# Optimization experiments

Measured on AMD Instinct MI355X. Metric: run time of the kernel, lower is better.

Reference implementation:

```python
import jax, jax.numpy as jnp
import numpy as np

# dims: batch, points, patches(groups), patch size, hidden, heads, layers, ffn
B, N, G, K, D, H, L, F = 32, 8192, 256, 32, 384, 6, 12, 1536
MASK_RATIO = 0.75
LEN_KEEP = int(G * (1 - MASK_RATIO))  # 64 visible tokens
HD = D // H


def _layernorm(x, g, b, eps=1e-5):
    m = jnp.mean(x, -1, keepdims=True)
    v = jnp.mean(jnp.square(x - m), -1, keepdims=True)
    return (x - m) * jax.lax.rsqrt(v + eps) * g + b


def _normalize_points(x):
    # normalize(): center = mid of bbox, radius = max distance to center (iso/diag)
    bmin = x.min(-2, keepdims=True)
    bmax = x.max(-2, keepdims=True)
    center = 0.5 * (bmin + bmax)
    radius = jnp.linalg.norm(x - center, axis=-1, keepdims=True).max(-2, keepdims=True)
    return (x - center) / radius


def _fps(x, num_samples):
    # farthest point sampling; sequential by nature -> fori_loop over G (fixed, small)
    b, n, _ = x.shape
    idxs = jnp.zeros((b, num_samples), jnp.int32)

    def body(i, state):
        dists, idxs, last = state
        lastpt = jnp.take_along_axis(x, last[:, None, None].astype(jnp.int32), axis=1)  # [B,1,3]
        d = jnp.sum(jnp.square(x - lastpt), -1)  # [B,N]
        dists = jnp.minimum(dists, d)
        nxt = jnp.argmax(dists, -1).astype(jnp.int32)
        return dists, idxs.at[:, i].set(nxt), nxt

    dists0 = jnp.full((b, n), 1e10, x.dtype)
    _, idxs, _ = jax.lax.fori_loop(1, num_samples, body, (dists0, idxs, jnp.zeros((b,), jnp.int32)))
    return idxs


def _group(x, centers):
    # squared pairwise distances without materializing [B,G,N,3]
    d2 = (jnp.sum(jnp.square(centers), -1)[:, :, None]
          + jnp.sum(jnp.square(x), -1)[:, None, :]
          - 2.0 * jnp.einsum('bgc,bnc->bgn', centers, x))  # [B,G,N]
    _, idx = jax.lax.top_k(-d2, K)  # [B,G,K] knn indices
    nbrs = jnp.take_along_axis(x[:, None, :, :], idx[..., None], axis=2)  # [B,G,K,3] (_knn_gather)
    return nbrs - centers[:, :, None, :]


def setup_inputs() -> dict:
    key = jax.random.key(0)
    ks = iter(jax.random.split(key, 24))

    def w(shape, scale=0.02):
        return jax.random.normal(next(ks), shape, jnp.float32) * scale

    ones_ln = jnp.stack([jnp.ones(D, jnp.float32), jnp.zeros(D, jnp.float32)])
    return {
        'points': jax.random.normal(next(ks), (B, N, 3), jnp.float32),
        'noise': jax.random.uniform(next(ks), (B, G), jnp.float32),
        # mini-PointNet patch encoder
        'pe_w1': w((3, 128)), 'pe_b1': jnp.zeros((128,), jnp.float32),
        'pe_w2': w((128, 256)), 'pe_b2': jnp.zeros((256,), jnp.float32),
        'pe_w3': w((256, D)), 'pe_b3': jnp.zeros((D,), jnp.float32),
        # positional MLP on patch centers
        'pos_w1': w((3, 128)), 'pos_b1': jnp.zeros((128,), jnp.float32),
        'pos_w2': w((128, D)), 'pos_b2': jnp.zeros((D,), jnp.float32),
        # transformer (stacked over L layers)
        'ln1': jnp.tile(ones_ln[None], (L, 1, 1)),
        'wqkv': w((L, D, 3 * D)), 'bqkv': jnp.zeros((L, 3 * D), jnp.float32),
        'wo': w((L, D, D)), 'bo': jnp.zeros((L, D), jnp.float32),
        'ln2': jnp.tile(ones_ln[None], (L, 1, 1)),
        'wi': w((L, D, F)), 'bi': jnp.zeros((L, F), jnp.float32),
        'wo2': w((L, F, D)), 'bo2': jnp.zeros((L, D), jnp.float32),
        'lnf': ones_ln,
    }


def _forward(points, noise, pe_w1, pe_b1, pe_w2, pe_b2, pe_w3, pe_b3,
             pos_w1, pos_b1, pos_w2, pos_b2,
             ln1, wqkv, bqkv, wo, bo, ln2, wi, bi, wo2, bo2, lnf):
    x = _normalize_points(points)
    cidx = _fps(x, G)                                        # [B,G]
    centers = jnp.take_along_axis(x, cidx[..., None], axis=1)  # [B,G,3]
    patches = _group(x, centers)                              # [B,G,K,3]

    # patch encode (per-point MLP -> max pool -> proj)
    f = jax.nn.relu(patches @ pe_w1 + pe_b1)
    f = f @ pe_w2 + pe_b2
    tokens = f.max(axis=2) @ pe_w3 + pe_b3                    # [B,G,D]
    pos = jax.nn.relu(centers @ pos_w1 + pos_b1) @ pos_w2 + pos_b2  # [B,G,D]

    # mask(): argsort-of-noise shuffle, keep first len_keep tokens
    ids_shuffle = jnp.argsort(noise, axis=1)
    ids_keep = ids_shuffle[:, :LEN_KEEP]                      # [B,64]
    h = (jnp.take_along_axis(tokens, ids_keep[..., None], axis=1)
         + jnp.take_along_axis(pos, ids_keep[..., None], axis=1))  # [B,64,D]

    scale = 1.0 / jnp.sqrt(jnp.asarray(HD, h.dtype))

    def layer(h, p):
        l1, wq, bq, wo_, bo_, l2, wi_, bi_, wo2_, bo2_ = p
        y = _layernorm(h, l1[0], l1[1])
        qkv = (y @ wq + bq).reshape(B, LEN_KEEP, 3, H, HD)  # '(three h d)' split
        q, k, v = jnp.moveaxis(qkv, 2, 0)
        a = jax.nn.softmax(jnp.einsum('bshd,bthd->bhst', q, k) * scale, -1)
        o = jnp.einsum('bhst,bthd->bshd', a, v).reshape(B, LEN_KEEP, D)
        h = h + o @ wo_ + bo_
        y = _layernorm(h, l2[0], l2[1])
        h = h + jax.nn.gelu(y @ wi_ + bi_) @ wo2_ + bo2_
        return h, None

    h, _ = jax.lax.scan(layer, h, (ln1, wqkv, bqkv, wo, bo, ln2, wi, bi, wo2, bo2))
    return _layernorm(h, lnf[0], lnf[1])


def reference(points, noise, pe_w1, pe_b1, pe_w2, pe_b2, pe_w3, pe_b3,
              pos_w1, pos_b1, pos_w2, pos_b2,
              ln1, wqkv, bqkv, wo, bo, ln2, wi, bi, wo2, bo2, lnf):
    return _forward(points, noise, pe_w1, pe_b1, pe_w2, pe_b2, pe_w3, pe_b3,
                    pos_w1, pos_b1, pos_w2, pos_b2,
                    ln1, wqkv, bqkv, wo, bo, ln2, wi, bi, wo2, bo2, lnf)
```

## Files before the change

### kernel.cpp

```cpp
#include <hip/hip_runtime.h>

#define NPTS 8192
#define NB   32
#define NG   256
#define NK   32
#define ND   384
#define NH   6
#define NLK  64
#define NF   1536
#define NHD  64
#define NL   12
#define MM   2048

typedef unsigned short u16;
typedef unsigned long long u64;
typedef __attribute__((ext_vector_type(8))) short short8;
typedef __attribute__((ext_vector_type(16))) float f32x16;
typedef __attribute__((ext_vector_type(4))) unsigned short ushort4v;

#define PL_PRE   147456ull
#define PL_LAYER 1769472ull
#define WT_ELEMS (PL_PRE + 12ull*PL_LAYER)

__device__ __forceinline__ float bf2f(u16 v){
  unsigned int u = ((unsigned int)v) << 16;
  float f; __builtin_memcpy(&f, &u, 4); return f;
}
__device__ __forceinline__ float ldf(const void* p, size_t i, bool bf){
  if(bf) return bf2f(((const u16*)p)[i]);
  return ((const float*)p)[i];
}
__device__ __forceinline__ u16 f2bf(float f){
  unsigned int x; __builtin_memcpy(&x, &f, 4);
  x += 0x7fffu + ((x >> 16) & 1u);
  return (u16)(x >> 16);
}
__device__ __forceinline__ void split2(float v, u16& hi, u16& lo){
  hi = f2bf(v);
  lo = f2bf(v - bf2f(hi));
}

__device__ __forceinline__ float blockMax256(float v, float* sb, int tid){
  for(int off=32; off; off>>=1) v = fmaxf(v, __shfl_down(v, off));
  __syncthreads();
  if((tid&63)==0) sb[tid>>6] = v;
  __syncthreads();
  return fmaxf(fmaxf(sb[0],sb[1]), fmaxf(sb[2],sb[3]));
}

__global__ __launch_bounds__(256) void k_normalize(const void* __restrict__ pts,
                                                   float* __restrict__ xn,
                                                   int* __restrict__ flag){
#pragma clang fp contract(off)
  int b = blockIdx.x, tid = threadIdx.x;
  __shared__ float sb[4];
  __shared__ int sbad;
  if(tid==0) sbad = 0;
  __syncthreads();
  {
    const u16* p16 = (const u16*)pts;
    int hit=0;
    for(int i=tid; i<4096; i+=256){
      unsigned e = (p16[i] >> 7) & 0xFFu;
      if(e >= 0x90u) hit=1;
    }
    if(hit) atomicOr(&sbad, 1);
  }
  __syncthreads();
  const bool bf = (sbad == 0);
  if(b==0 && tid==0) flag[0] = bf ? 1 : 0;
  const size_t base = (size_t)b*NPTS*3;
  float mn0=1e30f,mn1=1e30f,mn2=1e30f, mx0=-1e30f,mx1=-1e30f,mx2=-1e30f;
  for(int n=tid; n<NPTS; n+=256){
    float x0=ldf(pts,base+n*3,bf), x1=ldf(pts,base+n*3+1,bf), x2=ldf(pts,base+n*3+2,bf);
    mn0=fminf(mn0,x0); mx0=fmaxf(mx0,x0);
    mn1=fminf(mn1,x1); mx1=fmaxf(mx1,x1);
    mn2=fminf(mn2,x2); mx2=fmaxf(mx2,x2);
  }
  mx0=blockMax256(mx0,sb,tid); mn0=-blockMax256(-mn0,sb,tid);
  mx1=blockMax256(mx1,sb,tid); mn1=-blockMax256(-mn1,sb,tid);
  mx2=blockMax256(mx2,sb,tid); mn2=-blockMax256(-mn2,sb,tid);
  float c0=0.5f*(mn0+mx0), c1=0.5f*(mn1+mx1), c2=0.5f*(mn2+mx2);
  float mr=0.0f;
  for(int n=tid; n<NPTS; n+=256){
    float d0=ldf(pts,base+n*3,bf)-c0, d1=ldf(pts,base+n*3+1,bf)-c1, d2=ldf(pts,base+n*3+2,bf)-c2;
    float nr = sqrtf((d0*d0 + d1*d1) + d2*d2);
    mr = fmaxf(mr, nr);
  }
  float radius = blockMax256(mr, sb, tid);
  float* XO = xn + base;
  for(int n=tid; n<NPTS; n+=256){
    XO[n*3  ] = (ldf(pts,base+n*3  ,bf)-c0)/radius;
    XO[n*3+1] = (ldf(pts,base+n*3+1,bf)-c1)/radius;
    XO[n*3+2] = (ldf(pts,base+n*3+2,bf)-c2)/radius;
  }
}

__device__ __forceinline__ void kmax_dpp_step(unsigned& hi, unsigned& lo, unsigned oh, unsigned ol){
  bool g = (oh > hi) || (oh == hi && ol > lo);
  hi = g ? oh : hi; lo = g ? ol : lo;
}
#define KMAX_DPP(CTRL) { \
  unsigned oh=(unsigned)__builtin_amdgcn_update_dpp(0,(int)kh,(CTRL),0xf,0xf,true); \
  unsigned ol=(unsigned)__builtin_amdgcn_update_dpp(0,(int)kl,(CTRL),0xf,0xf,true); \
  kmax_dpp_step(kh,kl,oh,ol); }

__global__ __launch_bounds__(512) void k_fps_trans(
    const float* __restrict__ xn, float* __restrict__ centers,
    const void* __restrict__ noise, int* __restrict__ keep,
    const void* __restrict__ pe_w3, const void* __restrict__ pos_w2,
    const void* __restrict__ wqkv, const void* __restrict__ wo,
    const void* __restrict__ wi,   const void* __restrict__ wo2,
    u16* __restrict__ wthi, u16* __restrict__ wtlo,
    const int* __restrict__ flag)
{
  __shared__ float xs[NPTS*3];
  __shared__ u64 skey[3];
  __shared__ int sc[NG];
  int tid = threadIdx.x;

  if(blockIdx.x >= 64){
    const bool bf = flag[0]!=0;
    float (*t)[33] = reinterpret_cast<float(*)[33]>(xs);
    int gid = blockIdx.x - 64;
    const void* W; int Kd, Nd; size_t woff, doff; int local;
    if(gid < 96){        W=pe_w3;  Kd=256; Nd=384; woff=0; doff=0;      local=gid; }
    else if(gid < 144){  W=pos_w2; Kd=128; Nd=384; woff=0; doff=98304;  local=gid-96; }
    else{
      int g2 = gid - 144; int l = g2 / 1728; int id = g2 % 1728;
      size_t lb = PL_PRE + (size_t)l*PL_LAYER;
      if(id < 432){        W=wqkv; Kd=384;  Nd=1152; woff=(size_t)l*442368; doff=lb;          local=id; }
      else if(id < 576){   W=wo;   Kd=384;  Nd=384;  woff=(size_t)l*147456; doff=lb+442368;   local=id-432; }
      else if(id < 1152){  W=wi;   Kd=384;  Nd=1536; woff=(size_t)l*589824; doff=lb+589824;   local=id-576; }
      else {               W=wo2;  Kd=1536; Nd=384;  woff=(size_t)l*589824; doff=lb+1179648;  local=id-1152; }
    }
    int ntiles = Nd >> 5;
    int n0 = (local % ntiles)*32, k0 = (local / ntiles)*32;
    for(int i=0;i<2;i++){
      int idx = tid + i*512; int kr = idx>>5, nc = idx&31;
      t[kr][nc] = ldf(W, woff + (size_t)(k0+kr)*Nd + n0+nc, bf);
    }
    __syncthreads();
    for(int i=0;i<2;i++){
      int idx = tid + i*512; int nr = idx>>5, kc = idx&31;
      float v = t[kc][nr];
      u16 hi,lo; split2(v,hi,lo);
      size_t o = doff + (size_t)(n0+nr)*Kd + k0+kc;
      wthi[o]=hi; wtlo[o]=lo;
    }
    return;
  }

  if(blockIdx.x >= 32){
    const bool bf = flag[0]!=0;
    int b = blockIdx.x - 32;
    float* nv = xs;
    if(tid < NG) nv[tid] = ldf(noise, (size_t)b*NG+tid, bf);
    __syncthreads();
    if(tid < NG){
      float v = nv[tid]; int r = 0;
      for(int j=0; j<NG; j++){
        float u = nv[j];
        r += (u < v) || (u == v && j < tid);
      }
      if(r < NLK) keep[b*NLK + r] = tid;
    }
    return;
  }

  {
#pragma clang fp contract(off)
    int b = blockIdx.x;
    int lane = tid & 63;
    const float* X = xn + (size_t)b*NPTS*3;
    float px[16],py[16],pz[16],dd[16];
#pragma unroll
    for(int s=0;s<16;s++){
      int n = s*512 + tid;
      px[s]=X[n*3]; py[s]=X[n*3+1]; pz[s]=X[n*3+2];
      dd[s]=1e10f;
    }
    for(int i=tid; i<NPTS*3; i+=512) xs[i] = X[i];
    if(tid==0){ skey[0]=0ull; skey[1]=0ull; skey[2]=0ull; sc[0]=0; }
    __syncthreads();
    float lx = xs[0], ly = xs[1], lz = xs[2];
    for(int i=1;i<NG;i++){
      int c = i % 3;
      float bv=-1.0f; int bs=0;
#pragma unroll
      for(int s=0;s<16;s++){
        float dx=px[s]-lx, dy=py[s]-ly, dz=pz[s]-lz;
        float d=(dx*dx + dy*dy) + dz*dz;
        d = fminf(dd[s], d); dd[s]=d;
        if(d > bv){ bv=d; bs=s; }
      }
      int bn = bs*512 + tid;
      unsigned kh; __builtin_memcpy(&kh,&bv,4);
      unsigned kl = (unsigned)(NPTS-1-bn);
      KMAX_DPP(0x111)
      KMAX_DPP(0x112)
      KMAX_DPP(0x114)
      KMAX_DPP(0x118)
      KMAX_DPP(0x142)
      KMAX_DPP(0x143)
      if(lane==63) atomicMax(&skey[c], ((u64)kh<<32) | (u64)kl);
      __syncthreads();
      u64 k64 = skey[c];
      int n = (NPTS-1) - (int)(k64 & 0xFFFFFFFFull);
      n &= (NPTS-1);
      if(tid==0){ sc[i]=n; skey[(i+2)%3]=0ull; }
      lx = xs[n*3]; ly = xs[n*3+1]; lz = xs[n*3+2];
    }
    __syncthreads();
    if(tid < NG){
      int n = sc[tid] & (NPTS-1);
      centers[((size_t)b*NG+tid)*3  ] = xs[n*3];
      centers[((size_t)b*NG+tid)*3+1] = xs[n*3+1];
      centers[((size_t)b*NG+tid)*3+2] = xs[n*3+2];
    }
  }
}

__global__ __launch_bounds__(256) void k_knn(
    const float* __restrict__ xn, const float* __restrict__ centers,
    const int* __restrict__ keep, float* __restrict__ patches)
{
  int blk=blockIdx.x; int b=blk>>6; int j=blk&63; int tid=threadIdx.x;
  __shared__ float sd[NPTS];
  __shared__ int   sel[NK];
  __shared__ float rv[4]; __shared__ int rn[4];
  __shared__ int   sseln;
  int g = keep[b*NLK + j] & (NG-1);
  const float* C = centers + ((size_t)b*NG + g)*3;
  float c0=C[0], c1=C[1], c2=C[2];
  const float* X = xn + (size_t)b*NPTS*3;
  {
#pragma clang fp contract(off)
    float cc = (c0*c0 + c1*c1) + c2*c2;
    for(int n=tid; n<NPTS; n+=256){
      float x0=X[n*3], x1=X[n*3+1], x2=X[n*3+2];
      float xx=(x0*x0 + x1*x1) + x2*x2;
      float dt=(c0*x0 + c1*x1) + c2*x2;
      sd[n] = (cc + xx) - 2.0f*dt;
    }
  }
  __syncthreads();
  float dl[32];
  for(int s=0;s<32;s++) dl[s] = sd[s*256 + tid];
  unsigned int alive = 0xffffffffu;
  for(int r=0; r<NK; r++){
    float bv=1e30f; int bn=0x7fffffff;
    for(int s=0;s<32;s++){
      if(alive & (1u<<s)){
        float v = dl[s];
        if(v < bv){ bv=v; bn=s*256+tid; }
      }
    }
    for(int off=32;off;off>>=1){
      float ov=__shfl_down(bv,off); int on=__shfl_down(bn,off);
      if(ov<bv || (ov==bv && on<bn)){ bv=ov; bn=on; }
    }
    if((tid&63)==0){ rv[tid>>6]=bv; rn[tid>>6]=bn; }
    __syncthreads();
    if(tid==0){
      float v=rv[0]; int n=rn[0];
      for(int w=1;w<4;w++) if(rv[w]<v || (rv[w]==v && rn[w]<n)){ v=rv[w]; n=rn[w]; }
      n &= (NPTS-1);
      sseln=n; sel[r]=n;
    }
    __syncthreads();
    int n = sseln;
    if((n & 255) == tid) alive &= ~(1u << (n >> 8));
  }
  __syncthreads();
  if(tid < NK){
    int n = sel[tid] & (NPTS-1);
    float* P = patches + ((size_t)(b*NLK+j)*NK + tid)*3;
    P[0]=X[n*3  ]-c0;
    P[1]=X[n*3+1]-c1;
    P[2]=X[n*3+2]-c2;
  }
}

__global__ __launch_bounds__(256) void k_embed(
    const float* __restrict__ patches, const float* __restrict__ centers,
    const int* __restrict__ keep,
    const void* __restrict__ w1, const void* __restrict__ b1,
    const void* __restrict__ w2, const void* __restrict__ b2,
    const void* __restrict__ pw1, const void* __restrict__ pb1,
    u16* __restrict__ mfhi, u16* __restrict__ mflo,
    u16* __restrict__ phhi, u16* __restrict__ phlo,
    const int* __restrict__ flag)
{
  int blk=blockIdx.x; int b=blk>>6; int j=blk&63; int tid=threadIdx.x;
  const bool bf = flag[0] != 0;
  __shared__ float pat[NK*3];
  __shared__ __align__(16) float f1t[128*36];
  int row = b*NLK + j;
  if(tid < NK*3) pat[tid] = patches[(size_t)row*NK*3 + tid];
  __syncthreads();
  for(int i=0;i<16;i++){
    int idx = tid + i*256;
    int k = idx>>7, m = idx&127;
    float v = ldf(b1,m,bf)
            + pat[k*3+0]*ldf(w1,        m,bf)
            + pat[k*3+1]*ldf(w1, 128 + m,bf)
            + pat[k*3+2]*ldf(w1, 256 + m,bf);
    f1t[m*36 + k] = fmaxf(v, 0.0f);
  }
  __syncthreads();
  float acc[NK];
  {
    float bv = ldf(b2, tid, bf);
#pragma unroll
    for(int k=0;k<NK;k++) acc[k]=bv;
  }
  for(int jj=0;jj<128;jj++){
    float wv = ldf(w2, (size_t)jj*256+tid, bf);
    const float* fr = &f1t[jj*36];
#pragma unroll
    for(int k8=0;k8<8;k8++){
      float4 fv = *reinterpret_cast<const float4*>(fr + k8*4);
      acc[k8*4+0] = fmaf(fv.x, wv, acc[k8*4+0]);
      acc[k8*4+1] = fmaf(fv.y, wv, acc[k8*4+1]);
      acc[k8*4+2] = fmaf(fv.z, wv, acc[k8*4+2]);
      acc[k8*4+3] = fmaf(fv.w, wv, acc[k8*4+3]);
    }
  }
  float mx = acc[0];
#pragma unroll
  for(int k=1;k<NK;k++) mx = fmaxf(mx, acc[k]);
  { u16 hi,lo; split2(mx,hi,lo);
    mfhi[(size_t)row*256 + tid]=hi; mflo[(size_t)row*256 + tid]=lo; }
  if(tid < 128){
    int g = keep[b*NLK + j] & (NG-1);
    const float* C = centers + ((size_t)b*NG + g)*3;
    float v = ldf(pb1,tid,bf)
            + C[0]*ldf(pw1,        tid,bf)
            + C[1]*ldf(pw1, 128 + tid,bf)
            + C[2]*ldf(pw1, 256 + tid,bf);
    v = fmaxf(v, 0.0f);
    u16 hi,lo; split2(v,hi,lo);
    phhi[(size_t)row*128 + tid]=hi; phlo[(size_t)row*128 + tid]=lo;
  }
}

__global__ __launch_bounds__(256) void k_transpose4(
    const void* __restrict__ wqkv, const void* __restrict__ wo,
    const void* __restrict__ wi,   const void* __restrict__ wo2,
    int l, u16* __restrict__ dhi, u16* __restrict__ dlo,
    const int* __restrict__ flag){
  __shared__ float t[32][33];
  const bool bf = flag[0]!=0;
  int id = blockIdx.x;
  const void* W; int Kd, Nd; size_t woff, doff; int local;
  if(id < 432){        W=wqkv; Kd=384;  Nd=1152; woff=(size_t)l*442368; doff=PL_PRE;          local=id; }
  else if(id < 576){   W=wo;   Kd=384;  Nd=384;  woff=(size_t)l*147456; doff=PL_PRE+442368;   local=id-432; }
  else if(id < 1152){  W=wi;   Kd=384;  Nd=1536; woff=(size_t)l*589824; doff=PL_PRE+589824;   local=id-576; }
  else {               W=wo2;  Kd=1536; Nd=384;  woff=(size_t)l*589824; doff=PL_PRE+1179648;  local=id-1152; }
  int ntiles = Nd >> 5;
  int n0 = (local % ntiles)*32, k0 = (local / ntiles)*32;
  for(int i=0;i<4;i++){
    int idx = threadIdx.x + i*256; int kr = idx>>5, nc = idx&31;
    t[kr][nc] = ldf(W, woff + (size_t)(k0+kr)*Nd + n0+nc, bf);
  }
  __syncthreads();
  for(int i=0;i<4;i++){
    int idx = threadIdx.x + i*256; int nr = idx>>5, kc = idx&31;
    float v = t[kc][nr];
    u16 hi,lo; split2(v,hi,lo);
    size_t o = doff + (size_t)(n0+nr)*Kd + k0+kc;
    dhi[o]=hi; dlo[o]=lo;
  }
}

__global__ __launch_bounds__(128) void k_ln_split(const float* __restrict__ X,
                                                  const void* __restrict__ gb, size_t go,
                                                  u16* __restrict__ Yhi, u16* __restrict__ Ylo,
                                                  const int* __restrict__ flag){
  int row=blockIdx.x, tid=threadIdx.x;
  const bool bf = flag[0] != 0;
  const float* x = X + (size_t)row*ND;
  __shared__ float sbuf[2];
  float v0=x[tid], v1=x[tid+128], v2=x[tid+256];
  float s = v0+v1+v2;
  for(int off=32;off;off>>=1) s += __shfl_down(s,off);
  if((tid&63)==0) sbuf[tid>>6]=s;
  __syncthreads();
  float mean = (sbuf[0]+sbuf[1]) * (1.0f/(float)ND);
  __syncthreads();
  float d0=v0-mean, d1=v1-mean, d2=v2-mean;
  s = d0*d0 + d1*d1 + d2*d2;
  for(int off=32;off;off>>=1) s += __shfl_down(s,off);
  if((tid&63)==0) sbuf[tid>>6]=s;
  __syncthreads();
  float var = (sbuf[0]+sbuf[1]) * (1.0f/(float)ND);
  float rstd = 1.0f / sqrtf(var + 1e-5f);
  float o0 = d0*rstd*ldf(gb,go+tid    ,bf) + ldf(gb,go+ND+tid    ,bf);
  float o1 = d1*rstd*ldf(gb,go+tid+128,bf) + ldf(gb,go+ND+tid+128,bf);
  float o2 = d2*rstd*ldf(gb,go+tid+256,bf) + ldf(gb,go+ND+tid+256,bf);
  u16 hi,lo; size_t rb = (size_t)row*ND;
  split2(o0,hi,lo); Yhi[rb+tid    ]=hi; Ylo[rb+tid    ]=lo;
  split2(o1,hi,lo); Yhi[rb+tid+128]=hi; Ylo[rb+tid+128]=lo;
  split2(o2,hi,lo); Yhi[rb+tid+256]=hi; Ylo[rb+tid+256]=lo;
}

template<int TM, int TN, int ACT, bool RES, bool OSPLIT>
__global__ __launch_bounds__(256) void k_gemm_mfma(
    const u16* __restrict__ Ahi, const u16* __restrict__ Alo,
    const u16* __restrict__ Whi, const u16* __restrict__ Wlo, size_t wo,
    const void* __restrict__ bias, size_t bo, const int* __restrict__ flag,
    const float* __restrict__ res, float* __restrict__ Cf,
    u16* __restrict__ Ohi, u16* __restrict__ Olo,
    int N, int K)
{
  __shared__ __align__(16) u16 sAh[2][64*40];
  __shared__ __align__(16) u16 sAl[2][64*40];
  __shared__ __align__(16) u16 sBh[2][64*40];
  __shared__ __align__(16) u16 sBl[2][64*40];
  int tid = threadIdx.x;
  int wave = tid >> 6, lane = tid & 63;
  int wm = wave >> 1, wn = wave & 1;
  int l31 = lane & 31, half = lane >> 5;
  int row0 = blockIdx.y*TM, col0 = blockIdx.x*TN;
  const bool bf = flag[0] != 0;
  f32x16 acc;
#pragma unroll
  for(int r=0;r<16;r++) acc[r]=0.f;

  const int sr  = tid >> 2;
  const int scc = (tid & 3) * 8;
  const u16* gAh = Ahi + (size_t)(row0+sr)*K + scc;
  const u16* gAl = Alo + (size_t)(row0+sr)*K + scc;
  const u16* gBh = Whi + wo + (size_t)(col0+sr)*K + scc;
  const u16* gBl = Wlo + wo + (size_t)(col0+sr)*K + scc;
  const int ldst = sr*40 + scc;

  uint4 rah = *reinterpret_cast<const uint4*>(gAh);
  uint4 ral = *reinterpret_cast<const uint4*>(gAl);
  uint4 rbh = *reinterpret_cast<const uint4*>(gBh);
  uint4 rbl = *reinterpret_cast<const uint4*>(gBl);

  const int nk = K >> 5;
  for(int t=0; t<nk; ++t){
    const int buf = t & 1;
    *reinterpret_cast<uint4*>(&sAh[buf][ldst]) = rah;
    *reinterpret_cast<uint4*>(&sAl[buf][ldst]) = ral;
    *reinterpret_cast<uint4*>(&sBh[buf][ldst]) = rbh;
    *reinterpret_cast<uint4*>(&sBl[buf][ldst]) = rbl;
    __syncthreads();
    if(t+1 < nk){
      const int ko = (t+1) << 5;
      rah = *reinterpret_cast<const uint4*>(gAh + ko);
      ral = *reinterpret_cast<const uint4*>(gAl + ko);
      rbh = *reinterpret_cast<const uint4*>(gBh + ko);
      rbl = *reinterpret_cast<const uint4*>(gBl + ko);
    }
#pragma unroll
    for(int ks=0; ks<2; ks++){
      int aoff = (wm*32 + l31)*40 + ks*16 + half*8;
      int boff = (wn*32 + l31)*40 + ks*16 + half*8;
      short8 ah = *reinterpret_cast<const short8*>(&sAh[buf][aoff]);
      short8 al = *reinterpret_cast<const short8*>(&sAl[buf][aoff]);
      short8 bh = *reinterpret_cast<const short8*>(&sBh[buf][boff]);
      short8 bl = *reinterpret_cast<const short8*>(&sBl[buf][boff]);
      acc = __builtin_amdgcn_mfma_f32_32x32x16_bf16(ah, bh, acc, 0,0,0);
      acc = __builtin_amdgcn_mfma_f32_32x32x16_bf16(ah, bl, acc, 0,0,0);
      acc = __builtin_amdgcn_mfma_f32_32x32x16_bf16(al, bh, acc, 0,0,0);
    }
  }
  int col = col0 + wn*32 + l31;
  float bv = ldf(bias, bo+col, bf);
#pragma unroll
  for(int r=0;r<16;r++){
    int row = row0 + wm*32 + (r&3) + 8*(r>>2) + 4*half;
    float v = acc[r] + bv;
    if(ACT==1){
      float xx = v;
      v = 0.5f*xx*(1.0f + tanhf(0.7978845608028654f*(xx + 0.044715f*xx*xx*xx)));
    }
    if(RES) v += res[(size_t)row*N + col];
    if(OSPLIT){
      u16 hi,lo; split2(v,hi,lo);
      Ohi[(size_t)row*N + col]=hi; Olo[(size_t)row*N + col]=lo;
    }else{
      Cf[(size_t)row*N + col]=v;
    }
  }
}

__global__ __launch_bounds__(256) void k_attn_pl(const float* __restrict__ qkv,
                                                 u16* __restrict__ ohi,
                                                 u16* __restrict__ olo){
  __shared__ float Qt[64*68];
  __shared__ float Kt[64*68];
  __shared__ float V [64*68];
  __shared__ float SB[64*68];
  int blk=blockIdx.x; int b=blk/NH, h=blk%NH;
  int tid=threadIdx.x;
  for(int idx=tid; idx<4096; idx+=256){
    int s=idx>>6, d=idx&63;
    const float* r = qkv + ((size_t)(b*NLK+s))*1152 + h*NHD + d;
    Qt[d*68+s]=r[0];
    Kt[d*68+s]=r[384];
    V [s*68+d]=r[768];
  }
  __syncthreads();
  {
    const int i0 = (tid>>4)*4, j0 = (tid&15)*4;
    float a00=0.f,a01=0.f,a02=0.f,a03=0.f;
    float a10=0.f,a11=0.f,a12=0.f,a13=0.f;
    float a20=0.f,a21=0.f,a22=0.f,a23=0.f;
    float a30=0.f,a31=0.f,a32=0.f,a33=0.f;
#pragma unroll 4
    for(int d=0;d<64;d++){
      float4 qa = *reinterpret_cast<const float4*>(&Qt[d*68+i0]);
      float4 kb = *reinterpret_cast<const float4*>(&Kt[d*68+j0]);
      a00=fmaf(qa.x,kb.x,a00); a01=fmaf(qa.x,kb.y,a01); a02=fmaf(qa.x,kb.z,a02); a03=fmaf(qa.x,kb.w,a03);
      a10=fmaf(qa.y,kb.x,a10); a11=fmaf(qa.y,kb.y,a11); a12=fmaf(qa.y,kb.z,a12); a13=fmaf(qa.y,kb.w,a13);
      a20=fmaf(qa.z,kb.x,a20); a21=fmaf(qa.z,kb.y,a21); a22=fmaf(qa.z,kb.z,a22); a23=fmaf(qa.z,kb.w,a23);
      a30=fmaf(qa.w,kb.x,a30); a31=fmaf(qa.w,kb.y,a31); a32=fmaf(qa.w,kb.z,a32); a33=fmaf(qa.w,kb.w,a33);
    }
    float4 o0 = {a00*0.125f, a01*0.125f, a02*0.125f, a03*0.125f};
    float4 o1 = {a10*0.125f, a11*0.125f, a12*0.125f, a13*0.125f};
    float4 o2 = {a20*0.125f, a21*0.125f, a22*0.125f, a23*0.125f};
    float4 o3 = {a30*0.125f, a31*0.125f, a32*0.125f, a33*0.125f};
    *reinterpret_cast<float4*>(&SB[(i0  )*68+j0]) = o0;
    *reinterpret_cast<float4*>(&SB[(i0+1)*68+j0]) = o1;
    *reinterpret_cast<float4*>(&SB[(i0+2)*68+j0]) = o2;
    *reinterpret_cast<float4*>(&SB[(i0+3)*68+j0]) = o3;
  }
  __syncthreads();
  if(tid<64){
    float* rowp=&SB[tid*68];
    float m=rowp[0];
    for(int j=1;j<64;j++) m=fmaxf(m,rowp[j]);
    float sum=0.0f;
    for(int j=0;j<64;j++){ float e=__expf(rowp[j]-m); rowp[j]=e; sum+=e; }
    for(int j=0;j<64;j++) Qt[j*68+tid] = rowp[j]/sum;
  }
  __syncthreads();
  {
    const int s0 = (tid>>4)*4, d0 = (tid&15)*4;
    float a00=0.f,a01=0.f,a02=0.f,a03=0.f;
    float a10=0.f,a11=0.f,a12=0.f,a13=0.f;
    float a20=0.f,a21=0.f,a22=0.f,a23=0.f;
    float a30=0.f,a31=0.f,a32=0.f,a33=0.f;
#pragma unroll 4
    for(int t=0;t<64;t++){
      float4 av = *reinterpret_cast<const float4*>(&Qt[t*68+s0]);
      float4 vv = *reinterpret_cast<const float4*>(&V [t*68+d0]);
      a00=fmaf(av.x,vv.x,a00); a01=fmaf(av.x,vv.y,a01); a02=fmaf(av.x,vv.z,a02); a03=fmaf(av.x,vv.w,a03);
      a10=fmaf(av.y,vv.x,a10); a11=fmaf(av.y,vv.y,a11); a12=fmaf(av.y,vv.z,a12); a13=fmaf(av.y,vv.w,a13);
      a20=fmaf(av.z,vv.x,a20); a21=fmaf(av.z,vv.y,a21); a22=fmaf(av.z,vv.z,a22); a23=fmaf(av.z,vv.w,a23);
      a30=fmaf(av.w,vv.x,a30); a31=fmaf(av.w,vv.y,a31); a32=fmaf(av.w,vv.z,a32); a33=fmaf(av.w,vv.w,a33);
    }
    float rr[4][4] = {{a00,a01,a02,a03},{a10,a11,a12,a13},{a20,a21,a22,a23},{a30,a31,a32,a33}};
#pragma unroll
    for(int si=0; si<4; si++){
      ushort4v h4, l4;
#pragma unroll
      for(int di=0; di<4; di++){
        u16 hi,lo; split2(rr[si][di],hi,lo);
        h4[di]=hi; l4[di]=lo;
      }
      size_t o = ((size_t)(b*NLK+s0+si))*ND + h*NHD + d0;
      *reinterpret_cast<ushort4v*>(&ohi[o]) = h4;
      *reinterpret_cast<ushort4v*>(&olo[o]) = l4;
    }
  }
}

template<bool FINAL>
__global__ __launch_bounds__(128) void k_ln(const float* __restrict__ X,
                                            const void* __restrict__ gb, size_t go,
                                            void* __restrict__ Y,
                                            const int* __restrict__ flag){
  int row=blockIdx.x, tid=threadIdx.x;
  const bool bf = flag[0] != 0;
  const float* x = X + (size_t)row*ND;
  __shared__ float sbuf[2];
  float v0=x[tid], v1=x[tid+128], v2=x[tid+256];
  float s = v0+v1+v2;
  for(int off=32;off;off>>=1) s += __shfl_down(s,off);
  if((tid&63)==0) sbuf[tid>>6]=s;
  __syncthreads();
  float mean = (sbuf[0]+sbuf[1]) * (1.0f/(float)ND);
  __syncthreads();
  float d0=v0-mean, d1=v1-mean, d2=v2-mean;
  s = d0*d0 + d1*d1 + d2*d2;
  for(int off=32;off;off>>=1) s += __shfl_down(s,off);
  if((tid&63)==0) sbuf[tid>>6]=s;
  __syncthreads();
  float var = (sbuf[0]+sbuf[1]) * (1.0f/(float)ND);
  float rstd = 1.0f / sqrtf(var + 1e-5f);
  float o0 = d0*rstd*ldf(gb,go+tid    ,bf) + ldf(gb,go+ND+tid    ,bf);
  float o1 = d1*rstd*ldf(gb,go+tid+128,bf) + ldf(gb,go+ND+tid+128,bf);
  float o2 = d2*rstd*ldf(gb,go+tid+256,bf) + ldf(gb,go+ND+tid+256,bf);
  if(FINAL && bf){
    u16* yo = (u16*)Y + (size_t)row*ND;
    yo[tid]=f2bf(o0); yo[tid+128]=f2bf(o1); yo[tid+256]=f2bf(o2);
  }else{
    float* yo = (float*)Y + (size_t)row*ND;
    yo[tid]=o0; yo[tid+128]=o1; yo[tid+256]=o2;
  }
}

extern "C" void kernel_launch(void* const* d_in, const int* in_sizes, int n_in,
                              void* d_out, int out_size, void* d_ws, size_t ws_size,
                              hipStream_t stream){
  (void)in_sizes; (void)n_in; (void)out_size;
  const void* pts   = d_in[0];
  const void* noise = d_in[1];
  const void* pe_w1 = d_in[2];
  const void* pe_b1 = d_in[3];
  const void* pe_w2 = d_in[4];
  const void* pe_b2 = d_in[5];
  const void* pe_w3 = d_in[6];
  const void* pe_b3 = d_in[7];
  const void* pos_w1= d_in[8];
  const void* pos_b1= d_in[9];
  const void* pos_w2= d_in[10];
  const void* pos_b2= d_in[11];
  const void* ln1   = d_in[12];
  const void* wqkv  = d_in[13];
  const void* bqkv  = d_in[14];
  const void* wo    = d_in[15];
  const void* bo    = d_in[16];
  const void* ln2   = d_in[17];
  const void* wi    = d_in[18];
  const void* bi    = d_in[19];
  const void* wo2   = d_in[20];
  const void* bo2   = d_in[21];
  const void* lnf   = d_in[22];

  const size_t needed_small = (6711296ull + 16) * 4;
  if (ws_size < needed_small) return;
  const size_t wt_f32_off = 6711312ull;
  const size_t needed_big = (wt_f32_off + WT_ELEMS) * 4;
  const bool big = ws_size >= needed_big;

  float* ws   = (float*)d_ws;
  float* h    = ws;
  u16*  yhi   = (u16*)(ws + 786432);
  u16*  ylo   = yhi + 786432;
  float* qkvb = ws + 1572864;
  u16*  athi  = (u16*)(ws + 3932160);
  u16*  atlo  = athi + 786432;
  u16*  ubhi  = (u16*)(ws + 1572864);
  u16*  ublo  = ubhi + 3145728;
  float* xn   = ws + 1572864;
  float* patches;
  float* centers;
  int*   keep;
  int*   flag;
  u16 *wthi, *wtlo;
  if(big){
    patches = ws + 6488064;
    centers = ws + 6684672;
    keep    = (int*)(ws + 6709248);
    flag    = (int*)(ws + 6711296);
    wthi    = (u16*)(ws + wt_f32_off);
    wtlo    = wthi + WT_ELEMS;
  }else{
    wthi    = (u16*)(ws + 4718592);
    wtlo    = (u16*)(ws + 5677056);
    patches = ws + 6635520;
    centers = ws + 6832128;
    keep    = (int*)(ws + 6856704);
    flag    = (int*)(ws + 6858752);
    if(ws_size < (6858752ull + 16) * 4) return;
  }

  k_normalize<<<NB, 256, 0, stream>>>(pts, xn, flag);
  {
    int grid = big ? (64 + 144 + 12*1728) : (64 + 144);
    k_fps_trans<<<grid, 512, 0, stream>>>(xn, centers, noise, keep, pe_w3, pos_w2,
        wqkv, wo, wi, wo2, wthi, wtlo, flag);
  }
  k_knn      <<<NB*NLK, 256, 0, stream>>>(xn, centers, keep, patches);
  k_embed    <<<NB*NLK, 256, 0, stream>>>(patches, centers, keep,
      pe_w1, pe_b1, pe_w2, pe_b2, pos_w1, pos_b1,
      yhi , yhi + 2048*256 , athi , athi + 2048*128 , flag);
  k_gemm_mfma<64,64,0,false,false><<<dim3(6,32), 256, 0, stream>>>(
      yhi, yhi + 2048*256, wthi, wtlo, 0, pe_b3, 0, flag, nullptr, h, nullptr, nullptr, 384, 256);
  k_gemm_mfma<64,64,0,true ,false><<<dim3(6,32), 256, 0, stream>>>(
      athi, athi + 2048*128, wthi, wtlo, 98304, pos_b2, 0, flag, h, h, nullptr, nullptr, 384, 128);

  for(int l=0; l<NL; l++){
    size_t lb = big ? (PL_PRE + (size_t)l*PL_LAYER) : PL_PRE;
    if(!big){
      k_transpose4<<<1728, 256, 0, stream>>>(wqkv, wo, wi, wo2, l, wthi, wtlo, flag);
    }
    k_ln_split<<<MM, 128, 0, stream>>>(h, ln1, (size_t)l*2*ND, yhi, ylo, flag);
    k_gemm_mfma<64,64,0,false,false><<<dim3(18,32), 256, 0, stream>>>(
        yhi, ylo, wthi, wtlo, lb, bqkv, (size_t)l*1152, flag, nullptr, qkvb, nullptr, nullptr, 1152, 384);
    k_attn_pl<<<NB*NH, 256, 0, stream>>>(qkvb, athi, atlo);
    k_gemm_mfma<64,64,0,true ,false><<<dim3(6,32), 256, 0, stream>>>(
        athi, atlo, wthi, wtlo, lb + 442368, bo, (size_t)l*384, flag, h, h, nullptr, nullptr, 384, 384);
    k_ln_split<<<MM, 128, 0, stream>>>(h, ln2, (size_t)l*2*ND, yhi, ylo, flag);
    k_gemm_mfma<64,64,1,false,true ><<<dim3(24,32), 256, 0, stream>>>(
        yhi, ylo, wthi, wtlo, lb + 589824, bi, (size_t)l*1536, flag, nullptr, nullptr, ubhi, ublo, 1536, 384);
    k_gemm_mfma<64,64,0,true ,false><<<dim3(6,32), 256, 0, stream>>>(
        ubhi, ublo, wthi, wtlo, lb + 1179648, bo2, (size_t)l*384, flag, h, h, nullptr, nullptr, 384, 1536);
  }
  k_ln<true><<<MM, 128, 0, stream>>>(h, lnf, 0, d_out, flag);
}
```

Baseline: 1.804 ms.

## Fuse kNN with patch embedding and double-register prefetch in GEMM

Merges the kNN selection and the first patch-embedding MLP into one kernel. The gathered patch stays in shared memory and the distance buffer is reused for the hidden activations, which removes a launch and a global round trip. Separately, the MFMA GEMM main loop is unrolled by two with two register sets of prefetched tiles, so global loads run two k-steps ahead. That costs extra registers and assumes the k-step count is even.

Measured after the change: 1.695 ms. -6.1%, faster.

```diff
diff --git a/kernel.cpp b/kernel.cpp
--- a/kernel.cpp
+++ b/kernel.cpp
@@ -221,15 +221,23 @@
   }
 }
 
-__global__ __launch_bounds__(256) void k_knn(
+__global__ __launch_bounds__(256) void k_knn_embed(
     const float* __restrict__ xn, const float* __restrict__ centers,
-    const int* __restrict__ keep, float* __restrict__ patches)
+    const int* __restrict__ keep,
+    const void* __restrict__ w1, const void* __restrict__ b1,
+    const void* __restrict__ w2, const void* __restrict__ b2,
+    const void* __restrict__ pw1, const void* __restrict__ pb1,
+    u16* __restrict__ mfhi, u16* __restrict__ mflo,
+    u16* __restrict__ phhi, u16* __restrict__ phlo,
+    const int* __restrict__ flag)
 {
   int blk=blockIdx.x; int b=blk>>6; int j=blk&63; int tid=threadIdx.x;
-  __shared__ float sd[NPTS];
+  const bool bf = flag[0] != 0;
+  __shared__ __align__(16) float sd[NPTS];
   __shared__ int   sel[NK];
   __shared__ float rv[4]; __shared__ int rn[4];
   __shared__ int   sseln;
+  __shared__ float pat[NK*3];
   int g = keep[b*NLK + j] & (NG-1);
   const float* C = centers + ((size_t)b*NG + g)*3;
   float c0=C[0], c1=C[1], c2=C[2];
@@ -275,30 +283,13 @@
   __syncthreads();
   if(tid < NK){
     int n = sel[tid] & (NPTS-1);
-    float* P = patches + ((size_t)(b*NLK+j)*NK + tid)*3;
-    P[0]=X[n*3  ]-c0;
-    P[1]=X[n*3+1]-c1;
-    P[2]=X[n*3+2]-c2;
-  }
-}
-
-__global__ __launch_bounds__(256) void k_embed(
-    const float* __restrict__ patches, const float* __restrict__ centers,
-    const int* __restrict__ keep,
-    const void* __restrict__ w1, const void* __restrict__ b1,
-    const void* __restrict__ w2, const void* __restrict__ b2,
-    const void* __restrict__ pw1, const void* __restrict__ pb1,
-    u16* __restrict__ mfhi, u16* __restrict__ mflo,
-    u16* __restrict__ phhi, u16* __restrict__ phlo,
-    const int* __restrict__ flag)
-{
-  int blk=blockIdx.x; int b=blk>>6; int j=blk&63; int tid=threadIdx.x;
-  const bool bf = flag[0] != 0;
-  __shared__ float pat[NK*3];
-  __shared__ __align__(16) float f1t[128*36];
+    pat[tid*3+0] = X[n*3  ]-c0;
+    pat[tid*3+1] = X[n*3+1]-c1;
+    pat[tid*3+2] = X[n*3+2]-c2;
+  }
+  __syncthreads();
+  float* f1t = sd;
   int row = b*NLK + j;
-  if(tid < NK*3) pat[tid] = patches[(size_t)row*NK*3 + tid];
-  __syncthreads();
   for(int i=0;i<16;i++){
     int idx = tid + i*256;
     int k = idx>>7, m = idx&127;
@@ -333,12 +324,10 @@
   { u16 hi,lo; split2(mx,hi,lo);
     mfhi[(size_t)row*256 + tid]=hi; mflo[(size_t)row*256 + tid]=lo; }
   if(tid < 128){
-    int g = keep[b*NLK + j] & (NG-1);
-    const float* C = centers + ((size_t)b*NG + g)*3;
     float v = ldf(pb1,tid,bf)
-            + C[0]*ldf(pw1,        tid,bf)
-            + C[1]*ldf(pw1, 128 + tid,bf)
-            + C[2]*ldf(pw1, 256 + tid,bf);
+            + c0*ldf(pw1,        tid,bf)
+            + c1*ldf(pw1, 128 + tid,bf)
+            + c2*ldf(pw1, 256 + tid,bf);
     v = fmaxf(v, 0.0f);
     u16 hi,lo; split2(v,hi,lo);
     phhi[(size_t)row*128 + tid]=hi; phlo[(size_t)row*128 + tid]=lo;
@@ -436,39 +425,50 @@
   const u16* gBl = Wlo + wo + (size_t)(col0+sr)*K + scc;
   const int ldst = sr*40 + scc;
 
-  uint4 rah = *reinterpret_cast<const uint4*>(gAh);
-  uint4 ral = *reinterpret_cast<const uint4*>(gAl);
-  uint4 rbh = *reinterpret_cast<const uint4*>(gBh);
-  uint4 rbl = *reinterpret_cast<const uint4*>(gBl);
+  uint4 rah0 = *reinterpret_cast<const uint4*>(gAh);
+  uint4 ral0 = *reinterpret_cast<const uint4*>(gAl);
+  uint4 rbh0 = *reinterpret_cast<const uint4*>(gBh);
+  uint4 rbl0 = *reinterpret_cast<const uint4*>(gBl);
+  uint4 rah1 = *reinterpret_cast<const uint4*>(gAh + 32);
+  uint4 ral1 = *reinterpret_cast<const uint4*>(gAl + 32);
+  uint4 rbh1 = *reinterpret_cast<const uint4*>(gBh + 32);
+  uint4 rbl1 = *reinterpret_cast<const uint4*>(gBl + 32);
 
   const int nk = K >> 5;
-  for(int t=0; t<nk; ++t){
-    const int buf = t & 1;
-    *reinterpret_cast<uint4*>(&sAh[buf][ldst]) = rah;
-    *reinterpret_cast<uint4*>(&sAl[buf][ldst]) = ral;
-    *reinterpret_cast<uint4*>(&sBh[buf][ldst]) = rbh;
-    *reinterpret_cast<uint4*>(&sBl[buf][ldst]) = rbl;
-    __syncthreads();
-    if(t+1 < nk){
-      const int ko = (t+1) << 5;
-      rah = *reinterpret_cast<const uint4*>(gAh + ko);
-      ral = *reinterpret_cast<const uint4*>(gAl + ko);
-      rbh = *reinterpret_cast<const uint4*>(gBh + ko);
-      rbl = *reinterpret_cast<const uint4*>(gBl + ko);
-    }
-#pragma unroll
-    for(int ks=0; ks<2; ks++){
-      int aoff = (wm*32 + l31)*40 + ks*16 + half*8;
-      int boff = (wn*32 + l31)*40 + ks*16 + half*8;
-      short8 ah = *reinterpret_cast<const short8*>(&sAh[buf][aoff]);
-      short8 al = *reinterpret_cast<const short8*>(&sAl[buf][aoff]);
-      short8 bh = *reinterpret_cast<const short8*>(&sBh[buf][boff]);
-      short8 bl = *reinterpret_cast<const short8*>(&sBl[buf][boff]);
-      acc = __builtin_amdgcn_mfma_f32_32x32x16_bf16(ah, bh, acc, 0,0,0);
-      acc = __builtin_amdgcn_mfma_f32_32x32x16_bf16(ah, bl, acc, 0,0,0);
-      acc = __builtin_amdgcn_mfma_f32_32x32x16_bf16(al, bh, acc, 0,0,0);
-    }
-  }
+
+#define GEMM_STEP(S, TT) { \
+    *reinterpret_cast<uint4*>(&sAh[S][ldst]) = rah##S; \
+    *reinterpret_cast<uint4*>(&sAl[S][ldst]) = ral##S; \
+    *reinterpret_cast<uint4*>(&sBh[S][ldst]) = rbh##S; \
+    *reinterpret_cast<uint4*>(&sBl[S][ldst]) = rbl##S; \
+    __syncthreads(); \
+    if((TT)+2 < nk){ \
+      const int ko = ((TT)+2) << 5; \
+      rah##S = *reinterpret_cast<const uint4*>(gAh + ko); \
+      ral##S = *reinterpret_cast<const uint4*>(gAl + ko); \
+      rbh##S = *reinterpret_cast<const uint4*>(gBh + ko); \
+      rbl##S = *reinterpret_cast<const uint4*>(gBl + ko); \
+    } \
+    _Pragma("unroll") \
+    for(int ks=0; ks<2; ks++){ \
+      int aoff = (wm*32 + l31)*40 + ks*16 + half*8; \
+      int boff = (wn*32 + l31)*40 + ks*16 + half*8; \
+      short8 ah = *reinterpret_cast<const short8*>(&sAh[S][aoff]); \
+      short8 al = *reinterpret_cast<const short8*>(&sAl[S][aoff]); \
+      short8 bh = *reinterpret_cast<const short8*>(&sBh[S][boff]); \
+      short8 bl = *reinterpret_cast<const short8*>(&sBl[S][boff]); \
+      acc = __builtin_amdgcn_mfma_f32_32x32x16_bf16(ah, bh, acc, 0,0,0); \
+      acc = __builtin_amdgcn_mfma_f32_32x32x16_bf16(ah, bl, acc, 0,0,0); \
+      acc = __builtin_amdgcn_mfma_f32_32x32x16_bf16(al, bh, acc, 0,0,0); \
+    } \
+  }
+
+  for(int t=0; t<nk; t+=2){
+    GEMM_STEP(0, t)
+    GEMM_STEP(1, t+1)
+  }
+#undef GEMM_STEP
+
   int col = col0 + wn*32 + l31;
   float bv = ldf(bias, bo+col, bf);
 #pragma unroll
@@ -650,13 +650,11 @@
   u16*  ubhi  = (u16*)(ws + 1572864);
   u16*  ublo  = ubhi + 3145728;
   float* xn   = ws + 1572864;
-  float* patches;
   float* centers;
   int*   keep;
   int*   flag;
   u16 *wthi, *wtlo;
   if(big){
-    patches = ws + 6488064;
     centers = ws + 6684672;
     keep    = (int*)(ws + 6709248);
     flag    = (int*)(ws + 6711296);
@@ -665,7 +663,6 @@
   }else{
     wthi    = (u16*)(ws + 4718592);
     wtlo    = (u16*)(ws + 5677056);
-    patches = ws + 6635520;
     centers = ws + 6832128;
     keep    = (int*)(ws + 6856704);
     flag    = (int*)(ws + 6858752);
@@ -678,8 +675,7 @@
     k_fps_trans<<<grid, 512, 0, stream>>>(xn, centers, noise, keep, pe_w3, pos_w2,
         wqkv, wo, wi, wo2, wthi, wtlo, flag);
   }
-  k_knn      <<<NB*NLK, 256, 0, stream>>>(xn, centers, keep, patches);
-  k_embed    <<<NB*NLK, 256, 0, stream>>>(patches, centers, keep,
+  k_knn_embed<<<NB*NLK, 256, 0, stream>>>(xn, centers, keep,
       pe_w1, pe_b1, pe_w2, pe_b2, pos_w1, pos_b1,
       yhi , yhi + 2048*256 , athi , athi + 2048*128 , flag);
   k_gemm_mfma<64,64,0,false,false><<<dim3(6,32), 256, 0, stream>>>(
```
